# Optimization experiments

Hardware: AMD Instinct MI355X
Metric: run time of the kernel (lower is better)

## Reference

```python
import jax, jax.numpy as jnp
import numpy as np

N, E, B = 50000, 800000, 512
D_IN = 128
H = [128, 128, 128, 256, 128]
OUT = 2


def setup_inputs() -> dict:
    key = jax.random.key(0)
    ks = jax.random.split(key, 24)

    def w(k, i, o):
        return (jax.random.normal(k, (i, o), jnp.float32) / np.sqrt(i)).astype(jnp.float32)

    x = jax.random.normal(ks[0], (N, D_IN), jnp.float32)
    edge_index = jax.random.randint(ks[1], (2, E), 0, N)
    batch = (jnp.arange(N) * B) // N  # sorted graph ids, every graph non-empty

    return {
        "x": x,
        "edge_index": edge_index,
        "batch": batch,
        # SAGEConv k: out = mean_aggr(x_j) @ Wl + bl + x @ Wr  (PyG default: bias on lin_l, none on lin_r)
        "Wl1": w(ks[2], D_IN, H[0]), "Wr1": w(ks[3], D_IN, H[0]), "bl1": jnp.zeros((H[0],), jnp.float32),
        "Wl2": w(ks[4], H[0], H[1]), "Wr2": w(ks[5], H[0], H[1]), "bl2": jnp.zeros((H[1],), jnp.float32),
        "Wl3": w(ks[6], H[1], H[2]), "Wr3": w(ks[7], H[1], H[2]), "bl3": jnp.zeros((H[2],), jnp.float32),
        "W_f1": w(ks[8], H[2], H[3]), "b_f1": jnp.zeros((H[3],), jnp.float32),
        "W_f2": w(ks[9], H[3], H[4]), "b_f2": jnp.zeros((H[4],), jnp.float32),
        "W_sm": w(ks[10], H[4], OUT), "b_sm": jnp.zeros((OUT,), jnp.float32),
        "W_news": w(ks[11], D_IN, OUT), "b_news": jnp.zeros((OUT,), jnp.float32),
        "W_cat": w(ks[12], 2 * OUT, 1), "b_cat": jnp.zeros((1,), jnp.float32),
    }


def _sage(x, src, dst, Wl, Wr, bl):
    # mean aggregation of source-node features onto destination nodes
    msg = x[src]                                                     # [E, d] gather
    s = jax.ops.segment_sum(msg, dst, num_segments=N)                # [N, d] scatter-add
    cnt = jax.ops.segment_sum(jnp.ones((src.shape[0],), x.dtype), dst, num_segments=N)
    mean = s / jnp.maximum(cnt, 1.0)[:, None]
    return mean @ Wl + bl + x @ Wr


def reference(x, edge_index, batch, Wl1, Wr1, bl1, Wl2, Wr2, bl2, Wl3, Wr3, bl3,
              W_f1, b_f1, W_f2, b_f2, W_sm, b_sm, W_news, b_news, W_cat, b_cat):
    src, dst = edge_index[0], edge_index[1]
    h = jax.nn.relu(_sage(x, src, dst, Wl1, Wr1, bl1))
    h = jax.nn.relu(_sage(h, src, dst, Wl2, Wr2, bl2))
    h = jax.nn.relu(_sage(h, src, dst, Wl3, Wr3, bl3))

    h = jax.ops.segment_max(h, batch, num_segments=B)                # global_max_pool -> [B, H2]
    h = jax.nn.relu(h @ W_f1 + b_f1)
    h = jax.nn.relu(h @ W_f2 + b_f2)
    h = jax.nn.relu(h @ W_sm + b_sm)                                 # [B, OUT]

    # root = first node index of each graph (batch is sorted)
    root = jax.ops.segment_min(jnp.arange(N), batch, num_segments=B)  # [B]
    news = jax.nn.relu(x[root] @ W_news + b_news)                    # [B, OUT]

    out = jnp.concatenate([h, news], axis=-1) @ W_cat + b_cat        # [B, 1]
    return jax.nn.sigmoid(out)
```

## Files before the change

kernel.cpp:

```cpp
#include <hip/hip_runtime.h>
#include <hip/hip_bf16.h>
#include <math.h>

#define D 128
#define SA 144

typedef __attribute__((ext_vector_type(8))) short bf16x8;
typedef __attribute__((ext_vector_type(4))) float f32x4;

static __device__ __forceinline__ short f2b(float f) {
    unsigned u = __builtin_bit_cast(unsigned, f);
    unsigned r = (u + 0x7FFFu + ((u >> 16) & 1u)) >> 16;
    return (short)r;
}
static __device__ __forceinline__ float b2f(short b) {
    unsigned u = ((unsigned)(unsigned short)b) << 16;
    return __builtin_bit_cast(float, u);
}


struct PrepArgs {
    const float* x; short* xb; int total4; int xb_blocks;
    const float* w[6]; short* wo[6]; int w_blocks;
    const int* dst; int* bcnt; int E;
};

__global__ __launch_bounds__(256) void prep_kernel(PrepArgs a) {
    int bid = blockIdx.x, tid = threadIdx.x;
    if (bid < a.xb_blocks) {
        int idx = bid * 256 + tid;
        if (idx < a.total4) {
            float4 v = ((const float4*)a.x)[idx];
            short4 o;
            o.x = f2b(v.x); o.y = f2b(v.y); o.z = f2b(v.z); o.w = f2b(v.w);
            ((short4*)a.xb)[idx] = o;
        }
        return;
    }
    if (bid < a.xb_blocks + a.w_blocks) {
        int idx4 = (bid - a.xb_blocks) * 256 + tid;
        int base = idx4 * 4;
        int m = base >> 14;
        int i = base & 16383;
        const float* W = a.w[m];
        short* O = a.wo[m];
        int k = i >> 7, nn = i & 127;
        float4 v = *(const float4*)(W + k * D + nn);
        O[(nn + 0) * D + k] = f2b(v.x);
        O[(nn + 1) * D + k] = f2b(v.y);
        O[(nn + 2) * D + k] = f2b(v.z);
        O[(nn + 3) * D + k] = f2b(v.w);
        return;
    }
    __shared__ int hist[512];
    hist[tid] = 0; hist[tid + 256] = 0;
    __syncthreads();
    int e0 = (bid - a.xb_blocks - a.w_blocks) * 4096;
#pragma unroll
    for (int i = 0; i < 16; ++i) {
        int e = e0 + i * 256 + tid;
        if (e < a.E) atomicAdd(&hist[a.dst[e] >> 7], 1);
    }
    __syncthreads();
    int c = hist[tid];       if (c) atomicAdd(&a.bcnt[tid], c);
    c = hist[tid + 256];     if (c) atomicAdd(&a.bcnt[tid + 256], c);
}


__global__ __launch_bounds__(256) void scan512_kernel(const int* __restrict__ bcnt,
                                                      int* __restrict__ gbase,
                                                      int* __restrict__ gcursor) {
    __shared__ int sc[256];
    int tid = threadIdx.x;
    int a0 = bcnt[2 * tid], a1 = bcnt[2 * tid + 1];
    int s = a0 + a1;
    sc[tid] = s;
    __syncthreads();
    for (int off = 1; off < 256; off <<= 1) {
        int t = (tid >= off) ? sc[tid - off] : 0;
        __syncthreads();
        sc[tid] += t;
        __syncthreads();
    }
    int ex = sc[tid] - s;
    gbase[2 * tid] = ex;          gcursor[2 * tid] = ex;
    gbase[2 * tid + 1] = ex + a0; gcursor[2 * tid + 1] = ex + a0;
    if (tid == 255) gbase[512] = sc[255];
}


#define EPB 4096
__global__ __launch_bounds__(256) void bin_kernel(const int* __restrict__ src,
                                                  const int* __restrict__ dst,
                                                  int* __restrict__ gcursor,
                                                  unsigned* __restrict__ binned, int E) {
    __shared__ int hist[512];
    __shared__ int base[512];
    int tid = threadIdx.x;
    int e0 = blockIdx.x * EPB;
    hist[tid] = 0; hist[tid + 256] = 0;
    __syncthreads();
    unsigned pk[16]; int bv[16];
#pragma unroll
    for (int i = 0; i < 16; ++i) {
        int e = e0 + i * 256 + tid;
        if (e < E) {
            int s = src[e], d = dst[e];
            bv[i] = d >> 7;
            pk[i] = (unsigned)s | ((unsigned)(d & 127) << 25);
            atomicAdd(&hist[bv[i]], 1);
        } else bv[i] = -1;
    }
    __syncthreads();
    {
        int c0 = hist[tid];
        base[tid] = c0 ? atomicAdd(&gcursor[tid], c0) : 0;
        hist[tid] = 0;
        int c1 = hist[tid + 256];
        base[tid + 256] = c1 ? atomicAdd(&gcursor[tid + 256], c1) : 0;
        hist[tid + 256] = 0;
    }
    __syncthreads();
#pragma unroll
    for (int i = 0; i < 16; ++i) {
        if (bv[i] >= 0) {
            int off = atomicAdd(&hist[bv[i]], 1);
            binned[base[bv[i]] + off] = pk[i];
        }
    }
}


__global__ __launch_bounds__(256) void place_kernel(const unsigned* __restrict__ binned,
                                                    const int* __restrict__ gbase,
                                                    int* __restrict__ row_ptr,
                                                    float* __restrict__ inv_deg,
                                                    int* __restrict__ col,
                                                    int n, int E, int NB) {
    __shared__ int cnt[128];
    __shared__ int sc[128];
    __shared__ int cur[128];
    int b = blockIdx.x, tid = threadIdx.x;
    int node0 = b << 7;
    int node1 = node0 + 128; if (node1 > n) node1 = n;
    int start = gbase[b], end = gbase[b + 1];
    if (tid < 128) cnt[tid] = 0;
    __syncthreads();
    for (int i = start + tid; i < end; i += 256)
        atomicAdd(&cnt[binned[i] >> 25], 1);
    __syncthreads();
    if (tid < 128) sc[tid] = cnt[tid];
    __syncthreads();
    for (int off = 1; off < 128; off <<= 1) {
        int t = (tid < 128 && tid >= off) ? sc[tid - off] : 0;
        __syncthreads();
        if (tid < 128) sc[tid] += t;
        __syncthreads();
    }
    if (tid < 128) {
        int nd = node0 + tid;
        if (nd < node1) {
            int c = cnt[tid];
            int base = start + sc[tid] - c;
            row_ptr[nd] = base;
            inv_deg[nd] = 1.0f / (float)((c > 0) ? c : 1);
            cur[tid] = base;
        }
    }
    if (b == NB - 1 && tid == 0) row_ptr[n] = E;
    __syncthreads();
    for (int i = start + tid; i < end; i += 256) {
        unsigned e = binned[i];
        int pos = atomicAdd(&cur[e >> 25], 1);
        col[pos] = (int)(e & 0x01FFFFFFu);
    }
}


__global__ __launch_bounds__(256) void agg_kernel(
        const short* __restrict__ h, const int* __restrict__ row_ptr,
        const int* __restrict__ col, const float* __restrict__ inv_deg,
        short* __restrict__ out, int n) {
    int w = (blockIdx.x * blockDim.x + threadIdx.x) >> 6;
    int lane = threadIdx.x & 63;
    if (w >= n) return;
    int s = row_ptr[w], e = row_ptr[w + 1];
    int g = lane >> 4, l16 = lane & 15;
    float acc[8];
#pragma unroll
    for (int q = 0; q < 8; ++q) acc[q] = 0.f;
    int p = s + g;
    for (; p + 12 < e; p += 16) {
        int j0 = col[p];
        int j1 = col[p + 4];
        int j2 = col[p + 8];
        int j3 = col[p + 12];
        bf16x8 v0 = *(const bf16x8*)(h + (size_t)j0 * D + l16 * 8);
        bf16x8 v1 = *(const bf16x8*)(h + (size_t)j1 * D + l16 * 8);
        bf16x8 v2 = *(const bf16x8*)(h + (size_t)j2 * D + l16 * 8);
        bf16x8 v3 = *(const bf16x8*)(h + (size_t)j3 * D + l16 * 8);
#pragma unroll
        for (int q = 0; q < 8; ++q) acc[q] += b2f(v0[q]);
#pragma unroll
        for (int q = 0; q < 8; ++q) acc[q] += b2f(v1[q]);
#pragma unroll
        for (int q = 0; q < 8; ++q) acc[q] += b2f(v2[q]);
#pragma unroll
        for (int q = 0; q < 8; ++q) acc[q] += b2f(v3[q]);
    }
    for (; p < e; p += 4) {
        int j = col[p];
        bf16x8 v = *(const bf16x8*)(h + (size_t)j * D + l16 * 8);
#pragma unroll
        for (int q = 0; q < 8; ++q) acc[q] += b2f(v[q]);
    }
#pragma unroll
    for (int q = 0; q < 8; ++q) {
        acc[q] += __shfl_xor(acc[q], 16, 64);
        acc[q] += __shfl_xor(acc[q], 32, 64);
    }
    if (g == 0) {
        float sc = inv_deg[w];
        bf16x8 o;
#pragma unroll
        for (int q = 0; q < 8; ++q) o[q] = f2b(acc[q] * sc);
        *(bf16x8*)(out + (size_t)w * D + l16 * 8) = o;
    }
}


__global__ __launch_bounds__(256) void sage_mm_mfma(
        const short* __restrict__ Aagg, const short* __restrict__ Hin,
        const short* __restrict__ WlT,  const short* __restrict__ WrT,
        const float* __restrict__ bl,   short* __restrict__ out, int M) {
    __shared__ short lA[128 * SA];
    __shared__ short lW[128 * SA];
    int tid  = threadIdx.x;
    int wave = tid >> 6, lane = tid & 63;
    int row0 = blockIdx.x * 128;
    int mrow = wave * 32;
    int m16  = lane & 15, quad = lane >> 4;

    f32x4 acc[2][8];
#pragma unroll
    for (int i = 0; i < 2; ++i)
#pragma unroll
        for (int j = 0; j < 8; ++j) acc[i][j] = (f32x4){0.f, 0.f, 0.f, 0.f};

#pragma unroll
    for (int half = 0; half < 2; ++half) {
        const short* A = half ? Hin : Aagg;
        const short* W = half ? WrT : WlT;
#pragma unroll
        for (int it = 0; it < 8; ++it) {
            int idx = it * 256 + tid;
            int r = idx >> 4, c8 = (idx & 15) << 3;
            bf16x8 va = {0, 0, 0, 0, 0, 0, 0, 0};
            int gr = row0 + r;
            if (gr < M) va = *(const bf16x8*)(A + (size_t)gr * D + c8);
            *(bf16x8*)(&lA[r * SA + c8]) = va;
            bf16x8 vw = *(const bf16x8*)(W + r * D + c8);
            *(bf16x8*)(&lW[r * SA + c8]) = vw;
        }
        __syncthreads();
#pragma unroll
        for (int ks = 0; ks < 4; ++ks) {
            int kb = ks * 32 + quad * 8;
            bf16x8 a0 = *(const bf16x8*)(&lA[(mrow +      m16) * SA + kb]);
            bf16x8 a1 = *(const bf16x8*)(&lA[(mrow + 16 + m16) * SA + kb]);
#pragma unroll
            for (int nt = 0; nt < 8; ++nt) {
                bf16x8 b = *(const bf16x8*)(&lW[(nt * 16 + m16) * SA + kb]);
                acc[0][nt] = __builtin_amdgcn_mfma_f32_16x16x32_bf16(a0, b, acc[0][nt], 0, 0, 0);
                acc[1][nt] = __builtin_amdgcn_mfma_f32_16x16x32_bf16(a1, b, acc[1][nt], 0, 0, 0);
            }
        }
        __syncthreads();
    }
#pragma unroll
    for (int mt = 0; mt < 2; ++mt) {
#pragma unroll
        for (int r = 0; r < 4; ++r) {
            int grow = row0 + mrow + mt * 16 + quad * 4 + r;
            if (grow < M) {
#pragma unroll
                for (int nt = 0; nt < 8; ++nt) {
                    int gcol = nt * 16 + m16;
                    float v = acc[mt][nt][r] + bl[gcol];
                    out[(size_t)grow * D + gcol] = f2b(fmaxf(v, 0.f));
                }
            }
        }
    }
}


__global__ __launch_bounds__(256) void poolhead_kernel(
        const short* __restrict__ h, const int* __restrict__ batch,
        const float* __restrict__ x,
        const float* __restrict__ W_f1, const float* __restrict__ b_f1,
        const float* __restrict__ W_f2, const float* __restrict__ b_f2,
        const float* __restrict__ W_sm, const float* __restrict__ b_sm,
        const float* __restrict__ W_news, const float* __restrict__ b_news,
        const float* __restrict__ W_cat, const float* __restrict__ b_cat,
        float* __restrict__ out, int n) {
    int g = blockIdx.x;
    int tid = threadIdx.x;
    int f = tid & 127, half = tid >> 7;
    __shared__ float pm[256];
    __shared__ float p[128], t1[256], t2[128], hs[2], nw[2];
    int lo = 0, hi = n;
    while (lo < hi) { int m = (lo + hi) >> 1; if (batch[m] < g) lo = m + 1; else hi = m; }
    int start = lo;
    hi = n;
    while (lo < hi) { int m = (lo + hi) >> 1; if (batch[m] < g + 1) lo = m + 1; else hi = m; }
    int end = lo;
    float m = -3.4e38f;
    for (int i = start + half; i < end; i += 2) m = fmaxf(m, b2f(h[(size_t)i * D + f]));
    pm[tid] = m;
    __syncthreads();
    if (tid < 128) p[tid] = fmaxf(pm[tid], pm[tid + 128]);
    __syncthreads();
    float a1 = b_f1[tid];
    for (int k = 0; k < 128; ++k) a1 += p[k] * W_f1[k * 256 + tid];
    t1[tid] = fmaxf(a1, 0.f);
    __syncthreads();
    if (tid < 128) {
        float a2 = b_f2[tid];
        for (int k = 0; k < 256; ++k) a2 += t1[k] * W_f2[k * 128 + tid];
        t2[tid] = fmaxf(a2, 0.f);
    }
    __syncthreads();
    if (tid < 2) {
        float a3 = b_sm[tid];
        for (int k = 0; k < 128; ++k) a3 += t2[k] * W_sm[k * 2 + tid];
        hs[tid] = fmaxf(a3, 0.f);
        const float* xr = x + (size_t)start * D;
        float a4 = b_news[tid];
        for (int k = 0; k < 128; ++k) a4 += xr[k] * W_news[k * 2 + tid];
        nw[tid] = fmaxf(a4, 0.f);
    }
    __syncthreads();
    if (tid == 0) {
        float o = b_cat[0] + hs[0] * W_cat[0] + hs[1] * W_cat[1]
                           + nw[0] * W_cat[2] + nw[1] * W_cat[3];
        out[g] = 1.0f / (1.0f + __expf(-o));
    }
}


extern "C" void kernel_launch(void* const* d_in, const int* in_sizes, int n_in,
                              void* d_out, int out_size, void* d_ws, size_t ws_size,
                              hipStream_t stream) {
    const float* x      = (const float*)d_in[0];
    const int*   edge   = (const int*)d_in[1];
    const int*   batch  = (const int*)d_in[2];
    const float* Wl1 = (const float*)d_in[3];
    const float* Wr1 = (const float*)d_in[4];
    const float* bl1 = (const float*)d_in[5];
    const float* Wl2 = (const float*)d_in[6];
    const float* Wr2 = (const float*)d_in[7];
    const float* bl2 = (const float*)d_in[8];
    const float* Wl3 = (const float*)d_in[9];
    const float* Wr3 = (const float*)d_in[10];
    const float* bl3 = (const float*)d_in[11];
    const float* W_f1 = (const float*)d_in[12];
    const float* b_f1 = (const float*)d_in[13];
    const float* W_f2 = (const float*)d_in[14];
    const float* b_f2 = (const float*)d_in[15];
    const float* W_sm = (const float*)d_in[16];
    const float* b_sm = (const float*)d_in[17];
    const float* W_news = (const float*)d_in[18];
    const float* b_news = (const float*)d_in[19];
    const float* W_cat = (const float*)d_in[20];
    const float* b_cat = (const float*)d_in[21];
    float* out = (float*)d_out;

    const int E = in_sizes[1] / 2;
    const int n = in_sizes[2];
    const int B = out_size;

    const int* src = edge;
    const int* dst = edge + E;

    char* ws = (char*)d_ws;
    size_t off = 0;
    auto carve = [&](size_t bytes) {
        void* pt = ws + off;
        off = (off + bytes + 255) & ~(size_t)255;
        return pt;
    };
    int*      row_ptr = (int*)carve((size_t)(n + 1) * 4);
    float*    inv_deg = (float*)carve((size_t)n * 4);
    int*      col     = (int*)carve((size_t)E * 4);
    int*      bcnt    = (int*)carve((size_t)512 * 4);
    int*      gbase   = (int*)carve((size_t)513 * 4);
    int*      gcursor = (int*)carve((size_t)512 * 4);
    unsigned* binned  = (unsigned*)carve((size_t)E * 4);
    short*    xb      = (short*)carve((size_t)n * D * 2);
    short*    aggb    = (short*)carve((size_t)n * D * 2);
    short*    hA      = (short*)carve((size_t)n * D * 2);
    short*    hB      = (short*)carve((size_t)n * D * 2);
    short* Wt[6];
    for (int i = 0; i < 6; ++i) Wt[i] = (short*)carve((size_t)D * D * 2);
    (void)ws_size;

    hipMemsetAsync(bcnt, 0, 512 * 4, stream);
    PrepArgs pa;
    pa.x = x; pa.xb = xb; pa.total4 = n * D / 4;
    pa.xb_blocks = (pa.total4 + 255) / 256;
    pa.w[0] = Wl1; pa.w[1] = Wr1; pa.w[2] = Wl2; pa.w[3] = Wr2; pa.w[4] = Wl3; pa.w[5] = Wr3;
    for (int i = 0; i < 6; ++i) pa.wo[i] = Wt[i];
    pa.w_blocks = (6 * D * D) / 1024;
    pa.dst = dst; pa.bcnt = bcnt; pa.E = E;
    int h_blocks = (E + 4095) / 4096;
    prep_kernel<<<pa.xb_blocks + pa.w_blocks + h_blocks, 256, 0, stream>>>(pa);

    int NB = (n + 127) / 128;
    scan512_kernel<<<1, 256, 0, stream>>>(bcnt, gbase, gcursor);
    bin_kernel<<<(E + EPB - 1) / EPB, 256, 0, stream>>>(src, dst, gcursor, binned, E);
    place_kernel<<<NB, 256, 0, stream>>>(binned, gbase, row_ptr, inv_deg, col, n, E, NB);

    int agg_blocks = (n * 64 + 255) / 256;
    int mm_blocks  = (n + 127) / 128;

    agg_kernel<<<agg_blocks, 256, 0, stream>>>(xb, row_ptr, col, inv_deg, aggb, n);
    sage_mm_mfma<<<mm_blocks, 256, 0, stream>>>(aggb, xb, Wt[0], Wt[1], bl1, hA, n);
    agg_kernel<<<agg_blocks, 256, 0, stream>>>(hA, row_ptr, col, inv_deg, aggb, n);
    sage_mm_mfma<<<mm_blocks, 256, 0, stream>>>(aggb, hA, Wt[2], Wt[3], bl2, hB, n);
    agg_kernel<<<agg_blocks, 256, 0, stream>>>(hB, row_ptr, col, inv_deg, aggb, n);
    sage_mm_mfma<<<mm_blocks, 256, 0, stream>>>(aggb, hB, Wt[4], Wt[5], bl3, hA, n);

    poolhead_kernel<<<B, 256, 0, stream>>>(hA, batch, x,
                                           W_f1, b_f1, W_f2, b_f2, W_sm, b_sm,
                                           W_news, b_news, W_cat, b_cat, out, n);
}
```

Before: 312.9 us.

## Split neighbor aggregation into two feature-half passes to shrink gather working set

```diff
diff --git a/kernel.cpp b/kernel.cpp
--- a/kernel.cpp
+++ b/kernel.cpp
@@ -177,45 +177,39 @@
 }
 
 
-__global__ __launch_bounds__(256) void agg_kernel(
+__global__ __launch_bounds__(256) void agg_half_kernel(
         const short* __restrict__ h, const int* __restrict__ row_ptr,
         const int* __restrict__ col, const float* __restrict__ inv_deg,
-        short* __restrict__ out, int n) {
+        short* __restrict__ out, int n, int half) {
     int w = (blockIdx.x * blockDim.x + threadIdx.x) >> 6;
     int lane = threadIdx.x & 63;
     if (w >= n) return;
     int s = row_ptr[w], e = row_ptr[w + 1];
-    int g = lane >> 4, l16 = lane & 15;
+    int g = lane >> 3, l8 = lane & 7;
+    const short* hb = h + half * 64;
     float acc[8];
 #pragma unroll
     for (int q = 0; q < 8; ++q) acc[q] = 0.f;
     int p = s + g;
-    for (; p + 12 < e; p += 16) {
+    for (; p + 8 < e; p += 16) {
         int j0 = col[p];
-        int j1 = col[p + 4];
-        int j2 = col[p + 8];
-        int j3 = col[p + 12];
-        bf16x8 v0 = *(const bf16x8*)(h + (size_t)j0 * D + l16 * 8);
-        bf16x8 v1 = *(const bf16x8*)(h + (size_t)j1 * D + l16 * 8);
-        bf16x8 v2 = *(const bf16x8*)(h + (size_t)j2 * D + l16 * 8);
-        bf16x8 v3 = *(const bf16x8*)(h + (size_t)j3 * D + l16 * 8);
+        int j1 = col[p + 8];
+        bf16x8 v0 = *(const bf16x8*)(hb + (size_t)j0 * D + l8 * 8);
+        bf16x8 v1 = *(const bf16x8*)(hb + (size_t)j1 * D + l8 * 8);
 #pragma unroll
         for (int q = 0; q < 8; ++q) acc[q] += b2f(v0[q]);
 #pragma unroll
         for (int q = 0; q < 8; ++q) acc[q] += b2f(v1[q]);
-#pragma unroll
-        for (int q = 0; q < 8; ++q) acc[q] += b2f(v2[q]);
-#pragma unroll
-        for (int q = 0; q < 8; ++q) acc[q] += b2f(v3[q]);
-    }
-    for (; p < e; p += 4) {
+    }
+    if (p < e) {
         int j = col[p];
-        bf16x8 v = *(const bf16x8*)(h + (size_t)j * D + l16 * 8);
+        bf16x8 v = *(const bf16x8*)(hb + (size_t)j * D + l8 * 8);
 #pragma unroll
         for (int q = 0; q < 8; ++q) acc[q] += b2f(v[q]);
     }
 #pragma unroll
     for (int q = 0; q < 8; ++q) {
+        acc[q] += __shfl_xor(acc[q], 8, 64);
         acc[q] += __shfl_xor(acc[q], 16, 64);
         acc[q] += __shfl_xor(acc[q], 32, 64);
     }
@@ -224,7 +218,7 @@
         bf16x8 o;
 #pragma unroll
         for (int q = 0; q < 8; ++q) o[q] = f2b(acc[q] * sc);
-        *(bf16x8*)(out + (size_t)w * D + l16 * 8) = o;
+        *(bf16x8*)(out + (size_t)w * D + half * 64 + l8 * 8) = o;
     }
 }
 
@@ -424,11 +418,14 @@
     int agg_blocks = (n * 64 + 255) / 256;
     int mm_blocks  = (n + 127) / 128;
 
-    agg_kernel<<<agg_blocks, 256, 0, stream>>>(xb, row_ptr, col, inv_deg, aggb, n);
+    agg_half_kernel<<<agg_blocks, 256, 0, stream>>>(xb, row_ptr, col, inv_deg, aggb, n, 0);
+    agg_half_kernel<<<agg_blocks, 256, 0, stream>>>(xb, row_ptr, col, inv_deg, aggb, n, 1);
     sage_mm_mfma<<<mm_blocks, 256, 0, stream>>>(aggb, xb, Wt[0], Wt[1], bl1, hA, n);
-    agg_kernel<<<agg_blocks, 256, 0, stream>>>(hA, row_ptr, col, inv_deg, aggb, n);
+    agg_half_kernel<<<agg_blocks, 256, 0, stream>>>(hA, row_ptr, col, inv_deg, aggb, n, 0);
+    agg_half_kernel<<<agg_blocks, 256, 0, stream>>>(hA, row_ptr, col, inv_deg, aggb, n, 1);
     sage_mm_mfma<<<mm_blocks, 256, 0, stream>>>(aggb, hA, Wt[2], Wt[3], bl2, hB, n);
-    agg_kernel<<<agg_blocks, 256, 0, stream>>>(hB, row_ptr, col, inv_deg, aggb, n);
+    agg_half_kernel<<<agg_blocks, 256, 0, stream>>>(hB, row_ptr, col, inv_deg, aggb, n, 0);
+    agg_half_kernel<<<agg_blocks, 256, 0, stream>>>(hB, row_ptr, col, inv_deg, aggb, n, 1);
     sage_mm_mfma<<<mm_blocks, 256, 0, stream>>>(aggb, hB, Wt[4], Wt[5], bl3, hA, n);
 
     poolhead_kernel<<<B, 256, 0, stream>>>(hA, batch, x,
```

New measurement: 357.3 us. 1.14x slower.
